# Optimization experiments

Hardware: AMD Instinct MI355X
Metric: run time of the kernel (lower is better)

The kernel has to match this reference:

```python
import jax, jax.numpy as jnp
import numpy as np

N = 50000      # num_nodes
E = 1000000    # graph edges
EP = 400000    # pos/neg link-pred edges
H = 128        # hidden_dim
C = 768        # chemical_dim
L = 2          # num GCN layers


def setup_inputs() -> dict:
    key = jax.random.key(0)
    ks = jax.random.split(key, 12)
    edge_index = jax.random.randint(ks[0], (2, E), 0, N)
    chemistry = jax.random.normal(ks[1], (N, C), jnp.float32)
    pos_edge = jax.random.randint(ks[2], (EP, 2), 0, N)
    neg_edge = jax.random.randint(ks[3], (EP, 2), 0, N)
    smiles_mask = jax.random.uniform(ks[4], (N,), jnp.float32)
    node_emb = jax.random.normal(ks[5], (N, H), jnp.float32) * 0.1
    conv_w = jax.random.normal(ks[6], (L, H, H), jnp.float32) / np.sqrt(H)
    conv_b = jnp.zeros((L, H), jnp.float32)
    chem_w = jax.random.normal(ks[7], (C, H), jnp.float32) / np.sqrt(C)
    chem_b = jnp.zeros((H,), jnp.float32)
    dec_w1 = jax.random.normal(ks[8], (2 * H, H), jnp.float32) / np.sqrt(2 * H)
    dec_b1 = jnp.zeros((H,), jnp.float32)
    dec_w2 = jax.random.normal(ks[9], (H, 1), jnp.float32) / np.sqrt(H)
    dec_b2 = jnp.zeros((1,), jnp.float32)
    return dict(edge_index=edge_index, chemistry=chemistry, pos_edge=pos_edge,
                neg_edge=neg_edge, smiles_mask=smiles_mask, node_emb=node_emb,
                conv_w=conv_w, conv_b=conv_b, chem_w=chem_w, chem_b=chem_b,
                dec_w1=dec_w1, dec_b1=dec_b1, dec_w2=dec_w2, dec_b2=dec_b2)


def reference(edge_index, chemistry, pos_edge, neg_edge, smiles_mask, node_emb,
              conv_w, conv_b, chem_w, chem_b, dec_w1, dec_b1, dec_w2, dec_b2):
    row, col = edge_index[0], edge_index[1]  # src -> dst
    # GCN symmetric normalization (add_self_loops=False)
    deg = jax.ops.segment_sum(jnp.ones((E,), jnp.float32), col, num_segments=N)
    dinv = jnp.where(deg > 0, 1.0 / jnp.sqrt(jnp.maximum(deg, 1.0)), 0.0)
    norm = dinv[row] * dinv[col]  # [E]

    # Encoder: structure-only GCN over learned node embeddings
    z = node_emb
    for l in range(L):
        h = z @ conv_w[l]                       # [N,H]
        msg = h[row] * norm[:, None]            # gather [E,H]
        agg = jax.ops.segment_sum(msg, col, num_segments=N)  # scatter-add
        z = jax.nn.relu(agg + conv_b[l])

    # Chemistry projection, masked by smiles validity
    c = jax.nn.relu(chemistry @ chem_w + chem_b) * smiles_mask[:, None]  # [N,H]

    def decode(edges):
        src, dst = edges[:, 0], edges[:, 1]
        f = jnp.concatenate([z[src] * z[dst], c[src] * c[dst]], axis=-1)  # [Ep,2H]
        hmid = jax.nn.relu(f @ dec_w1 + dec_b1)
        return (hmid @ dec_w2 + dec_b2)[:, 0]

    return decode(pos_edge), decode(neg_edge)
```

## Files before the change

### kernel.cpp

```cpp
#include <hip/hip_runtime.h>
#include <hip/hip_fp16.h>

#define NN 50000
#define NE 1000000
#define NEP 400000
#define HD 128
#define CD 768
#define NB_SCAN 196
#define FSTR 256
#define NBKT 196
#define PBLK 2048
#define NPB ((2 * NEP + PBLK - 1) / PBLK)

typedef _Float16 f16x8 __attribute__((ext_vector_type(8)));
typedef _Float16 f16x2 __attribute__((ext_vector_type(2)));
typedef __fp16 hf16x2 __attribute__((ext_vector_type(2)));
typedef __attribute__((ext_vector_type(4))) float f32x4;

__device__ __forceinline__ unsigned pk2h(float a, float b) {
    hf16x2 p = __builtin_amdgcn_cvt_pkrtz(a, b);
    return __builtin_bit_cast(unsigned, p);
}
__device__ __forceinline__ ushort f2h(float x) {
    return (ushort)(pk2h(x, 0.f) & 0xffffu);
}
__device__ __forceinline__ unsigned h2mul(unsigned a, unsigned b) {
    f16x2 ha = __builtin_bit_cast(f16x2, a);
    f16x2 hb = __builtin_bit_cast(f16x2, b);
    f16x2 r = ha * hb;
    return __builtin_bit_cast(unsigned, r);
}
__device__ __forceinline__ f16x8 pack8h(float4 a0, float4 a1) {
    union { unsigned u[4]; f16x8 v; } r;
    r.u[0] = pk2h(a0.x, a0.y);
    r.u[1] = pk2h(a0.z, a0.w);
    r.u[2] = pk2h(a1.x, a1.y);
    r.u[3] = pk2h(a1.z, a1.w);
    return r.v;
}
__device__ __forceinline__ float2 h2f2(unsigned u) {
    f16x2 h = __builtin_bit_cast(f16x2, u);
    return make_float2((float)h[0], (float)h[1]);
}

__global__ __launch_bounds__(256) void count_kernel(const int* __restrict__ col,
                                                    int* __restrict__ cnt) {
    int i = blockIdx.x * 256 + threadIdx.x;
    if (i < NE) atomicAdd(&cnt[col[i]], 1);
}

__global__ __launch_bounds__(256) void dinv_kernel(const int* __restrict__ cnt,
                                                   float* __restrict__ dinv) {
    int i = blockIdx.x * 256 + threadIdx.x;
    if (i < NN) {
        int d = cnt[i];
        dinv[i] = (d > 0) ? 1.0f / sqrtf((float)d) : 0.0f;
    }
}

__global__ __launch_bounds__(256) void scan1_kernel(const int* __restrict__ cnt,
                                                    int* __restrict__ partial,
                                                    int* __restrict__ bsum) {
    __shared__ int s[256];
    int i = blockIdx.x * 256 + threadIdx.x;
    int v = (i < NN) ? cnt[i] : 0;
    s[threadIdx.x] = v;
    __syncthreads();
    for (int o = 1; o < 256; o <<= 1) {
        int t = (threadIdx.x >= o) ? s[threadIdx.x - o] : 0;
        __syncthreads();
        s[threadIdx.x] += t;
        __syncthreads();
    }
    if (i < NN) partial[i] = s[threadIdx.x] - v;
    if (threadIdx.x == 255) bsum[blockIdx.x] = s[255];
}

__global__ __launch_bounds__(256) void scan2_kernel(int* __restrict__ bsum) {
    __shared__ int s[256];
    int v = (threadIdx.x < NB_SCAN) ? bsum[threadIdx.x] : 0;
    s[threadIdx.x] = v;
    __syncthreads();
    for (int o = 1; o < 256; o <<= 1) {
        int t = (threadIdx.x >= o) ? s[threadIdx.x - o] : 0;
        __syncthreads();
        s[threadIdx.x] += t;
        __syncthreads();
    }
    if (threadIdx.x < NB_SCAN) bsum[threadIdx.x] = s[threadIdx.x] - v;
}

__global__ __launch_bounds__(256) void scan3_kernel(const int* __restrict__ partial,
                                                    const int* __restrict__ bsum,
                                                    int* __restrict__ off,
                                                    int* __restrict__ cursor) {
    int i = blockIdx.x * 256 + threadIdx.x;
    if (i < NN) {
        int o = partial[i] + bsum[blockIdx.x];
        off[i] = o;
        cursor[i] = o;
    }
}

__global__ __launch_bounds__(256) void fill_kernel(const int* __restrict__ row,
                                                   const int* __restrict__ col,
                                                   const float* __restrict__ dinv,
                                                   int* __restrict__ cursor,
                                                   int* __restrict__ csr_idx,
                                                   float* __restrict__ csr_w) {
    int e = blockIdx.x * 256 + threadIdx.x;
    if (e < NE) {
        int c = col[e], r = row[e];
        int slot = atomicAdd(&cursor[c], 1);
        csr_idx[slot] = r;
        csr_w[slot] = dinv[r];
    }
}

__global__ __launch_bounds__(256) void ehist_kernel(const int* __restrict__ pos,
                                                    const int* __restrict__ neg,
                                                    int* __restrict__ bh,
                                                    int* __restrict__ bcnt) {
    __shared__ int h[NBKT];
    const int t = threadIdx.x;
    if (t < NBKT) h[t] = 0;
    __syncthreads();
    const int base = blockIdx.x * PBLK;
#pragma unroll
    for (int j = 0; j < 8; ++j) {
        int i = base + t + j * 256;
        if (i < 2 * NEP) {
            int s = (i < NEP) ? pos[2 * i] : neg[2 * (i - NEP)];
            atomicAdd(&h[s >> 8], 1);
        }
    }
    __syncthreads();
    if (t < NBKT) {
        bh[blockIdx.x * NBKT + t] = h[t];
        if (h[t]) atomicAdd(&bcnt[t], h[t]);
    }
}

__global__ __launch_bounds__(256) void escan_kernel(const int* __restrict__ bcnt,
                                                    int* __restrict__ base) {
    __shared__ int s[256];
    const int t = threadIdx.x;
    int v = (t < NBKT) ? bcnt[t] : 0;
    s[t] = v;
    __syncthreads();
    for (int o = 1; o < 256; o <<= 1) {
        int x = (t >= o) ? s[t - o] : 0;
        __syncthreads();
        s[t] += x;
        __syncthreads();
    }
    if (t < NBKT) base[t] = s[t] - v;
}

__global__ __launch_bounds__(256) void bscan_kernel(const int* __restrict__ bh,
                                                    int* __restrict__ obh) {
    __shared__ int p[256];
    const int b = blockIdx.x;
    const int t = threadIdx.x;
    int v0 = (2 * t < NPB) ? bh[(size_t)(2 * t) * NBKT + b] : 0;
    int v1 = (2 * t + 1 < NPB) ? bh[(size_t)(2 * t + 1) * NBKT + b] : 0;
    p[t] = v0 + v1;
    __syncthreads();
    for (int o = 1; o < 256; o <<= 1) {
        int x = (t >= o) ? p[t - o] : 0;
        __syncthreads();
        p[t] += x;
        __syncthreads();
    }
    int excl = (t > 0) ? p[t - 1] : 0;
    if (2 * t < NPB) obh[(size_t)(2 * t) * NBKT + b] = excl;
    if (2 * t + 1 < NPB) obh[(size_t)(2 * t + 1) * NBKT + b] = excl + v0;
}

__global__ __launch_bounds__(256) void epermute_kernel(const int* __restrict__ pos,
                                                       const int* __restrict__ neg,
                                                       const int* __restrict__ base,
                                                       const int* __restrict__ obh,
                                                       uint2* __restrict__ sd,
                                                       int* __restrict__ oidx) {
    __shared__ int cur[NBKT];
    const int t = threadIdx.x;
    if (t < NBKT) cur[t] = base[t] + obh[(size_t)blockIdx.x * NBKT + t];
    __syncthreads();
    const int bb = blockIdx.x * PBLK;
#pragma unroll
    for (int j = 0; j < 8; ++j) {
        int i = bb + t + j * 256;
        if (i < 2 * NEP) {
            int s, d;
            if (i < NEP) { s = pos[2 * i]; d = pos[2 * i + 1]; }
            else { s = neg[2 * (i - NEP)]; d = neg[2 * (i - NEP) + 1]; }
            int slot = atomicAdd(&cur[s >> 8], 1);
            sd[slot] = make_uint2((unsigned)s, (unsigned)d);
            oidx[slot] = i;
        }
    }
}

__global__ __launch_bounds__(256) void wfrag_kernel(const float* __restrict__ w,
                                                    ushort* __restrict__ wf) {
    int tid = blockIdx.x * 256 + threadIdx.x;
    int ks = tid >> 9, nt = (tid >> 6) & 7, l = tid & 63;
    int kbase = ks * 32 + ((l >> 4) << 3);
    int colq = nt * 16 + (l & 15);
    ushort r[8];
#pragma unroll
    for (int j = 0; j < 8; ++j) r[j] = f2h(w[(size_t)(kbase + j) * HD + colq]);
    *(uint4*)&wf[(size_t)tid * 8] = *(uint4*)r;
}

template <int KS, bool EPI>
__global__ __launch_bounds__(256) void feat_mfma_kernel(const float* __restrict__ A,
                                                        const ushort* __restrict__ wf,
                                                        const float* __restrict__ bias,
                                                        const float* __restrict__ mask,
                                                        ushort* __restrict__ out,
                                                        int ostride, int ooff) {
    __shared__ float At[64][36];
    const int t = threadIdx.x;
    const int w = t >> 6, lane = t & 63;
    const int rowBase = blockIdx.x * 64;
    const int nt0 = w * 2;
    const int K = KS * 32;

    f32x4 acc[4][2] = {};

    for (int ks = 0; ks < KS; ++ks) {
        __syncthreads();
#pragma unroll
        for (int i = 0; i < 2; ++i) {
            int li = t + i * 256;
            int r = li >> 3, c4 = li & 7;
            int grow = rowBase + r;
            float4 v = make_float4(0.f, 0.f, 0.f, 0.f);
            if (grow < NN) v = *(const float4*)&A[(size_t)grow * K + ks * 32 + c4 * 4];
            *(float4*)&At[r][c4 * 4] = v;
        }
        __syncthreads();
        f16x8 bf0 = ((const f16x8*)wf)[(ks * 8 + nt0) * 64 + lane];
        f16x8 bf1 = ((const f16x8*)wf)[(ks * 8 + nt0 + 1) * 64 + lane];
#pragma unroll
        for (int mt = 0; mt < 4; ++mt) {
            int row = mt * 16 + (lane & 15);
            float4 a0 = *(const float4*)&At[row][(lane >> 4) * 8];
            float4 a1 = *(const float4*)&At[row][(lane >> 4) * 8 + 4];
            f16x8 af = pack8h(a0, a1);
            acc[mt][0] = __builtin_amdgcn_mfma_f32_16x16x32_f16(af, bf0, acc[mt][0], 0, 0, 0);
            acc[mt][1] = __builtin_amdgcn_mfma_f32_16x16x32_f16(af, bf1, acc[mt][1], 0, 0, 0);
        }
    }

    const int c0 = lane & 15, rq = lane >> 4;
    float bb0 = EPI ? bias[nt0 * 16 + c0] : 0.f;
    float bb1 = EPI ? bias[nt0 * 16 + 16 + c0] : 0.f;
#pragma unroll
    for (int mt = 0; mt < 4; ++mt) {
#pragma unroll
        for (int reg = 0; reg < 4; ++reg) {
            int grow = rowBase + mt * 16 + rq * 4 + reg;
            if (grow < NN) {
                float v0 = acc[mt][0][reg], v1 = acc[mt][1][reg];
                if (EPI) {
                    float m = mask[grow];
                    v0 = fmaxf(v0 + bb0, 0.f) * m;
                    v1 = fmaxf(v1 + bb1, 0.f) * m;
                }
                out[(size_t)grow * ostride + ooff + nt0 * 16 + c0] = f2h(v0);
                out[(size_t)grow * ostride + ooff + nt0 * 16 + 16 + c0] = f2h(v1);
            }
        }
    }
}

template <bool F16OUT>
__global__ __launch_bounds__(256) void gather_kernel(const int* __restrict__ off,
                                                     const int* __restrict__ cnt,
                                                     const int* __restrict__ csr_idx,
                                                     const float* __restrict__ csr_w,
                                                     const float* __restrict__ dinv,
                                                     const ushort* __restrict__ h,
                                                     const float* __restrict__ bias,
                                                     float* __restrict__ z,
                                                     ushort* __restrict__ zb,
                                                     int ostride) {
    int v = blockIdx.x * 4 + (threadIdx.x >> 6);
    if (v >= NN) return;
    int lane = threadIdx.x & 63;
    int s = off[v];
    int e = s + cnt[v];
    float accx = 0.f, accy = 0.f;
    for (; s + 7 < e; s += 8) {
        int r0 = csr_idx[s], r1 = csr_idx[s + 1], r2 = csr_idx[s + 2], r3 = csr_idx[s + 3];
        int r4 = csr_idx[s + 4], r5 = csr_idx[s + 5], r6 = csr_idx[s + 6], r7 = csr_idx[s + 7];
        unsigned u0 = *(const unsigned*)&h[(size_t)r0 * HD + lane * 2];
        unsigned u1 = *(const unsigned*)&h[(size_t)r1 * HD + lane * 2];
        unsigned u2 = *(const unsigned*)&h[(size_t)r2 * HD + lane * 2];
        unsigned u3 = *(const unsigned*)&h[(size_t)r3 * HD + lane * 2];
        unsigned u4 = *(const unsigned*)&h[(size_t)r4 * HD + lane * 2];
        unsigned u5 = *(const unsigned*)&h[(size_t)r5 * HD + lane * 2];
        unsigned u6 = *(const unsigned*)&h[(size_t)r6 * HD + lane * 2];
        unsigned u7 = *(const unsigned*)&h[(size_t)r7 * HD + lane * 2];
        float w0 = csr_w[s], w1 = csr_w[s + 1], w2 = csr_w[s + 2], w3 = csr_w[s + 3];
        float w4 = csr_w[s + 4], w5 = csr_w[s + 5], w6 = csr_w[s + 6], w7 = csr_w[s + 7];
        float2 f0 = h2f2(u0), f1 = h2f2(u1), f2 = h2f2(u2), f3 = h2f2(u3);
        float2 f4 = h2f2(u4), f5 = h2f2(u5), f6 = h2f2(u6), f7 = h2f2(u7);
        accx = fmaf(f0.x, w0, accx); accy = fmaf(f0.y, w0, accy);
        accx = fmaf(f1.x, w1, accx); accy = fmaf(f1.y, w1, accy);
        accx = fmaf(f2.x, w2, accx); accy = fmaf(f2.y, w2, accy);
        accx = fmaf(f3.x, w3, accx); accy = fmaf(f3.y, w3, accy);
        accx = fmaf(f4.x, w4, accx); accy = fmaf(f4.y, w4, accy);
        accx = fmaf(f5.x, w5, accx); accy = fmaf(f5.y, w5, accy);
        accx = fmaf(f6.x, w6, accx); accy = fmaf(f6.y, w6, accy);
        accx = fmaf(f7.x, w7, accx); accy = fmaf(f7.y, w7, accy);
    }
    for (; s < e; ++s) {
        int r0 = csr_idx[s];
        float w0 = csr_w[s];
        float2 f0 = h2f2(*(const unsigned*)&h[(size_t)r0 * HD + lane * 2]);
        accx = fmaf(f0.x, w0, accx); accy = fmaf(f0.y, w0, accy);
    }
    float dv = dinv[v];
    float2 b = *(const float2*)&bias[lane * 2];
    float ox = fmaxf(fmaf(accx, dv, b.x), 0.f);
    float oy = fmaxf(fmaf(accy, dv, b.y), 0.f);
    if (F16OUT) {
        *(unsigned*)&zb[(size_t)v * ostride + lane * 2] = pk2h(ox, oy);
    } else {
        float2 o; o.x = ox; o.y = oy;
        *(float2*)&z[(size_t)v * HD + lane * 2] = o;
    }
}

__global__ __launch_bounds__(256, 4) void decode_mfma_kernel(const uint2* __restrict__ sedges,
                                                             const int* __restrict__ soidx,
                                                             const ushort* __restrict__ feat,
                                                             const ushort* __restrict__ w1f,
                                                             const float* __restrict__ b1,
                                                             const float* __restrict__ w2,
                                                             const float* __restrict__ b2,
                                                             float* __restrict__ out) {
    __shared__ ushort Flds[8 * 4 * 64 * 8];
    __shared__ int sEdge[128];
    __shared__ int sOut[64];
    __shared__ float part[4][64];
    const int t = threadIdx.x;
    const int w = t >> 6, lane = t & 63;

    const int nwg = gridDim.x;
    const int orig = blockIdx.x;
    const int q = nwg >> 3, r = nwg & 7;
    const int xcd = orig & 7, k = orig >> 3;
    const int wgid = (xcd < r ? xcd * (q + 1) : r * (q + 1) + (xcd - r) * q) + k;
    const int ebase = wgid * 64;

    if (t < 128) sEdge[t] = ((const int*)sedges)[(size_t)ebase * 2 + t];
    if (t < 64) sOut[t] = soidx[ebase + t];
    __syncthreads();

    const int seg = t & 31, eslot = t >> 5;
#pragma unroll
    for (int it = 0; it < 8; ++it) {
        int e = it * 8 + eslot;
        int s = sEdge[2 * e], dd = sEdge[2 * e + 1];
        uint4 av = *(const uint4*)&feat[(size_t)s * FSTR + seg * 8];
        uint4 bv = *(const uint4*)&feat[(size_t)dd * FSTR + seg * 8];
        uint4 res;
        res.x = h2mul(av.x, bv.x);
        res.y = h2mul(av.y, bv.y);
        res.z = h2mul(av.z, bv.z);
        res.w = h2mul(av.w, bv.w);
        int ks = seg >> 2;
        int mt = e >> 4;
        int fl = (e & 15) | ((seg & 3) << 4);
        int swz = (seg & 3) | ((ks & 1) << 2);
        ((uint4*)Flds)[(ks * 4 + mt) * 64 + (fl ^ swz)] = res;
    }
    __syncthreads();

    f32x4 acc[4][2] = {};
    const int nt0 = w * 2;
#pragma unroll
    for (int ks = 0; ks < 8; ++ks) {
        f16x8 bf0 = ((const f16x8*)w1f)[(ks * 8 + nt0) * 64 + lane];
        f16x8 bf1 = ((const f16x8*)w1f)[(ks * 8 + nt0 + 1) * 64 + lane];
        const int rswz = ((lane >> 4) & 3) | ((ks & 1) << 2);
#pragma unroll
        for (int mt = 0; mt < 4; ++mt) {
            f16x8 af = ((const f16x8*)Flds)[(ks * 4 + mt) * 64 + (lane ^ rswz)];
            acc[mt][0] = __builtin_amdgcn_mfma_f32_16x16x32_f16(af, bf0, acc[mt][0], 0, 0, 0);
            acc[mt][1] = __builtin_amdgcn_mfma_f32_16x16x32_f16(af, bf1, acc[mt][1], 0, 0, 0);
        }
    }

    const int c0 = lane & 15, rq = lane >> 4;
    float b1v0 = b1[nt0 * 16 + c0], b1v1 = b1[nt0 * 16 + 16 + c0];
    float w2v0 = w2[nt0 * 16 + c0], w2v1 = w2[nt0 * 16 + 16 + c0];
#pragma unroll
    for (int mt = 0; mt < 4; ++mt) {
#pragma unroll
        for (int reg = 0; reg < 4; ++reg) {
            float h0 = fmaxf(acc[mt][0][reg] + b1v0, 0.f);
            float h1 = fmaxf(acc[mt][1][reg] + b1v1, 0.f);
            float p = fmaf(h0, w2v0, h1 * w2v1);
            p += __shfl_xor(p, 1);
            p += __shfl_xor(p, 2);
            p += __shfl_xor(p, 4);
            p += __shfl_xor(p, 8);
            if (c0 == 0) part[w][mt * 16 + rq * 4 + reg] = p;
        }
    }
    __syncthreads();
    if (t < 64) {
        out[sOut[t]] = part[0][t] + part[1][t] + part[2][t] + part[3][t] + b2[0];
    }
}

extern "C" void kernel_launch(void* const* d_in, const int* in_sizes, int n_in,
                              void* d_out, int out_size, void* d_ws, size_t ws_size,
                              hipStream_t stream) {
    const int* edge_index = (const int*)d_in[0];
    const float* chemistry = (const float*)d_in[1];
    const int* pos_edge = (const int*)d_in[2];
    const int* neg_edge = (const int*)d_in[3];
    const float* smiles_mask = (const float*)d_in[4];
    const float* node_emb = (const float*)d_in[5];
    const float* conv_w = (const float*)d_in[6];
    const float* conv_b = (const float*)d_in[7];
    const float* chem_w = (const float*)d_in[8];
    const float* chem_b = (const float*)d_in[9];
    const float* dec_w1 = (const float*)d_in[10];
    const float* dec_b1 = (const float*)d_in[11];
    const float* dec_w2 = (const float*)d_in[12];
    const float* dec_b2 = (const float*)d_in[13];
    float* out = (float*)d_out;

    char* ws = (char*)d_ws;
    int* cnt = (int*)(ws + 0);
    float* dinv = (float*)(ws + 204800);
    int* partial = (int*)(ws + 409600);
    int* off = (int*)(ws + 614400);
    int* cursor = (int*)(ws + 819200);
    int* bsum = (int*)(ws + 1024000);
    int* bcnt = (int*)(ws + 1025024);
    int* bbase = (int*)(ws + 1026048);
    int* csr_idx = (int*)(ws + 1048576);
    float* csr_w = (float*)(ws + 5242880);
    float* bufZ = (float*)(ws + 9437184);
    ushort* hb = (ushort*)(ws + 35037184);
    ushort* feat = (ushort*)(ws + 47837184);
    ushort* w1f = (ushort*)(ws + 73437184);
    ushort* wcf = (ushort*)(ws + 73502720);
    ushort* wc0f = (ushort*)(ws + 73699328);
    ushort* wc1f = (ushort*)(ws + 73732096);
    uint2* sort_sd = (uint2*)(ws + 35037184);
    int* sort_oidx = (int*)(ws + 41437184);
    int* bh = (int*)(ws + 9437184);
    int* obh = (int*)(ws + 9857184);

    const int* e_row = edge_index;
    const int* e_col = edge_index + NE;

    hipMemsetAsync(cnt, 0, (size_t)NN * 4, stream);
    hipMemsetAsync(bcnt, 0, NBKT * 4, stream);
    count_kernel<<<(NE + 255) / 256, 256, 0, stream>>>(e_col, cnt);
    dinv_kernel<<<(NN + 255) / 256, 256, 0, stream>>>(cnt, dinv);
    scan1_kernel<<<NB_SCAN, 256, 0, stream>>>(cnt, partial, bsum);
    scan2_kernel<<<1, 256, 0, stream>>>(bsum);
    scan3_kernel<<<NB_SCAN, 256, 0, stream>>>(partial, bsum, off, cursor);
    fill_kernel<<<(NE + 255) / 256, 256, 0, stream>>>(e_row, e_col, dinv, cursor, csr_idx, csr_w);
    wfrag_kernel<<<16, 256, 0, stream>>>(dec_w1, w1f);
    wfrag_kernel<<<48, 256, 0, stream>>>(chem_w, wcf);
    wfrag_kernel<<<8, 256, 0, stream>>>(conv_w, wc0f);
    wfrag_kernel<<<8, 256, 0, stream>>>(conv_w + HD * HD, wc1f);

    const int mmGrid = (NN + 63) / 64;
    const int gaGrid = (NN + 3) / 4;

    feat_mfma_kernel<4, false><<<mmGrid, 256, 0, stream>>>(node_emb, wc0f, nullptr, nullptr, hb, HD, 0);
    gather_kernel<false><<<gaGrid, 256, 0, stream>>>(off, cnt, csr_idx, csr_w, dinv, hb, conv_b, bufZ, nullptr, 0);

    feat_mfma_kernel<4, false><<<mmGrid, 256, 0, stream>>>(bufZ, wc1f, nullptr, nullptr, hb, HD, 0);
    gather_kernel<true><<<gaGrid, 256, 0, stream>>>(off, cnt, csr_idx, csr_w, dinv, hb, conv_b + HD, nullptr, feat, FSTR);

    ehist_kernel<<<NPB, 256, 0, stream>>>(pos_edge, neg_edge, bh, bcnt);
    escan_kernel<<<1, 256, 0, stream>>>(bcnt, bbase);
    bscan_kernel<<<NBKT, 256, 0, stream>>>(bh, obh);
    epermute_kernel<<<NPB, 256, 0, stream>>>(pos_edge, neg_edge, bbase, obh, sort_sd, sort_oidx);

    feat_mfma_kernel<24, true><<<mmGrid, 256, 0, stream>>>(chemistry, wcf, chem_b, smiles_mask, feat, FSTR, HD);

    decode_mfma_kernel<<<2 * NEP / 64, 256, 0, stream>>>(sort_sd, sort_oidx, feat, w1f,
                                                         dec_b1, dec_w2, dec_b2, out);
}
```

Before: 452.7 us.

## Merge setup kernels, double-buffer feature GEMM loads, trim decode shared memory

Folds the dinv computation into the first scan kernel, merges the four weight-fragment conversions into one launch, and collapses two memsets into one by moving bcnt next to cnt. The feature GEMM now double-buffers its A tile in LDS and prefetches the next K-slice into registers, which removes one barrier per iteration. The decode kernel drops its shared edge and output-index staging, reads edges directly from global memory, reuses Flds for the partial sums, and raises its occupancy hint to 5. These aim to cut launch overhead and memory stalls, at the cost of more register pressure in decode and twice the LDS in the GEMM.

```diff
diff --git a/kernel.cpp b/kernel.cpp
--- a/kernel.cpp
+++ b/kernel.cpp
@@ -49,21 +49,14 @@
     if (i < NE) atomicAdd(&cnt[col[i]], 1);
 }
 
-__global__ __launch_bounds__(256) void dinv_kernel(const int* __restrict__ cnt,
-                                                   float* __restrict__ dinv) {
-    int i = blockIdx.x * 256 + threadIdx.x;
-    if (i < NN) {
-        int d = cnt[i];
-        dinv[i] = (d > 0) ? 1.0f / sqrtf((float)d) : 0.0f;
-    }
-}
-
 __global__ __launch_bounds__(256) void scan1_kernel(const int* __restrict__ cnt,
                                                     int* __restrict__ partial,
-                                                    int* __restrict__ bsum) {
+                                                    int* __restrict__ bsum,
+                                                    float* __restrict__ dinv) {
     __shared__ int s[256];
     int i = blockIdx.x * 256 + threadIdx.x;
     int v = (i < NN) ? cnt[i] : 0;
+    if (i < NN) dinv[i] = (v > 0) ? 1.0f / sqrtf((float)v) : 0.0f;
     s[threadIdx.x] = v;
     __syncthreads();
     for (int o = 1; o < 256; o <<= 1) {
@@ -202,16 +195,30 @@
     }
 }
 
-__global__ __launch_bounds__(256) void wfrag_kernel(const float* __restrict__ w,
-                                                    ushort* __restrict__ wf) {
+__global__ __launch_bounds__(256) void wfrag_all_kernel(const float* __restrict__ w1,
+                                                        const float* __restrict__ wc,
+                                                        const float* __restrict__ w0,
+                                                        const float* __restrict__ wl1,
+                                                        ushort* __restrict__ w1f,
+                                                        ushort* __restrict__ wcf,
+                                                        ushort* __restrict__ wc0f,
+                                                        ushort* __restrict__ wc1f) {
     int tid = blockIdx.x * 256 + threadIdx.x;
-    int ks = tid >> 9, nt = (tid >> 6) & 7, l = tid & 63;
+    int g = tid >> 9;
+    const float* w;
+    ushort* wf;
+    int ks;
+    if (g < 8) { w = w1; wf = w1f; ks = g; }
+    else if (g < 32) { w = wc; wf = wcf; ks = g - 8; }
+    else if (g < 36) { w = w0; wf = wc0f; ks = g - 32; }
+    else { w = wl1; wf = wc1f; ks = g - 36; }
+    int nt = (tid >> 6) & 7, l = tid & 63;
     int kbase = ks * 32 + ((l >> 4) << 3);
     int colq = nt * 16 + (l & 15);
     ushort r[8];
 #pragma unroll
     for (int j = 0; j < 8; ++j) r[j] = f2h(w[(size_t)(kbase + j) * HD + colq]);
-    *(uint4*)&wf[(size_t)tid * 8] = *(uint4*)r;
+    *(uint4*)&wf[(size_t)((ks * 8 + nt) * 64 + l) * 8] = *(uint4*)r;
 }
 
 template <int KS, bool EPI>
@@ -221,34 +228,39 @@
                                                         const float* __restrict__ mask,
                                                         ushort* __restrict__ out,
                                                         int ostride, int ooff) {
-    __shared__ float At[64][36];
+    __shared__ float At[2][64][36];
     const int t = threadIdx.x;
     const int w = t >> 6, lane = t & 63;
     const int rowBase = blockIdx.x * 64;
     const int nt0 = w * 2;
     const int K = KS * 32;
 
+    const int sr0 = t >> 3, sr1 = 32 + (t >> 3), sc4 = (t & 7) * 4;
+    const int g0 = rowBase + sr0, g1 = rowBase + sr1;
+
+    float4 p0 = make_float4(0.f, 0.f, 0.f, 0.f), p1 = p0;
+    if (g0 < NN) p0 = *(const float4*)&A[(size_t)g0 * K + sc4];
+    if (g1 < NN) p1 = *(const float4*)&A[(size_t)g1 * K + sc4];
+
     f32x4 acc[4][2] = {};
 
     for (int ks = 0; ks < KS; ++ks) {
-        __syncthreads();
-#pragma unroll
-        for (int i = 0; i < 2; ++i) {
-            int li = t + i * 256;
-            int r = li >> 3, c4 = li & 7;
-            int grow = rowBase + r;
-            float4 v = make_float4(0.f, 0.f, 0.f, 0.f);
-            if (grow < NN) v = *(const float4*)&A[(size_t)grow * K + ks * 32 + c4 * 4];
-            *(float4*)&At[r][c4 * 4] = v;
-        }
-        __syncthreads();
+        const int b = ks & 1;
+        *(float4*)&At[b][sr0][sc4] = p0;
+        *(float4*)&At[b][sr1][sc4] = p1;
+        __syncthreads();
+        if (ks + 1 < KS) {
+            p0 = make_float4(0.f, 0.f, 0.f, 0.f); p1 = p0;
+            if (g0 < NN) p0 = *(const float4*)&A[(size_t)g0 * K + (ks + 1) * 32 + sc4];
+            if (g1 < NN) p1 = *(const float4*)&A[(size_t)g1 * K + (ks + 1) * 32 + sc4];
+        }
         f16x8 bf0 = ((const f16x8*)wf)[(ks * 8 + nt0) * 64 + lane];
         f16x8 bf1 = ((const f16x8*)wf)[(ks * 8 + nt0 + 1) * 64 + lane];
 #pragma unroll
         for (int mt = 0; mt < 4; ++mt) {
             int row = mt * 16 + (lane & 15);
-            float4 a0 = *(const float4*)&At[row][(lane >> 4) * 8];
-            float4 a1 = *(const float4*)&At[row][(lane >> 4) * 8 + 4];
+            float4 a0 = *(const float4*)&At[b][row][(lane >> 4) * 8];
+            float4 a1 = *(const float4*)&At[b][row][(lane >> 4) * 8 + 4];
             f16x8 af = pack8h(a0, a1);
             acc[mt][0] = __builtin_amdgcn_mfma_f32_16x16x32_f16(af, bf0, acc[mt][0], 0, 0, 0);
             acc[mt][1] = __builtin_amdgcn_mfma_f32_16x16x32_f16(af, bf1, acc[mt][1], 0, 0, 0);
@@ -336,7 +348,7 @@
     }
 }
 
-__global__ __launch_bounds__(256, 4) void decode_mfma_kernel(const uint2* __restrict__ sedges,
+__global__ __launch_bounds__(256, 5) void decode_mfma_kernel(const uint2* __restrict__ sedges,
                                                              const int* __restrict__ soidx,
                                                              const ushort* __restrict__ feat,
                                                              const ushort* __restrict__ w1f,
@@ -345,9 +357,6 @@
                                                              const float* __restrict__ b2,
                                                              float* __restrict__ out) {
     __shared__ ushort Flds[8 * 4 * 64 * 8];
-    __shared__ int sEdge[128];
-    __shared__ int sOut[64];
-    __shared__ float part[4][64];
     const int t = threadIdx.x;
     const int w = t >> 6, lane = t & 63;
 
@@ -358,17 +367,13 @@
     const int wgid = (xcd < r ? xcd * (q + 1) : r * (q + 1) + (xcd - r) * q) + k;
     const int ebase = wgid * 64;
 
-    if (t < 128) sEdge[t] = ((const int*)sedges)[(size_t)ebase * 2 + t];
-    if (t < 64) sOut[t] = soidx[ebase + t];
-    __syncthreads();
-
     const int seg = t & 31, eslot = t >> 5;
 #pragma unroll
     for (int it = 0; it < 8; ++it) {
         int e = it * 8 + eslot;
-        int s = sEdge[2 * e], dd = sEdge[2 * e + 1];
-        uint4 av = *(const uint4*)&feat[(size_t)s * FSTR + seg * 8];
-        uint4 bv = *(const uint4*)&feat[(size_t)dd * FSTR + seg * 8];
+        uint2 sd = sedges[ebase + e];
+        uint4 av = *(const uint4*)&feat[(size_t)sd.x * FSTR + seg * 8];
+        uint4 bv = *(const uint4*)&feat[(size_t)sd.y * FSTR + seg * 8];
         uint4 res;
         res.x = h2mul(av.x, bv.x);
         res.y = h2mul(av.y, bv.y);
@@ -396,7 +401,9 @@
             acc[mt][1] = __builtin_amdgcn_mfma_f32_16x16x32_f16(af, bf1, acc[mt][1], 0, 0, 0);
         }
     }
-
+    __syncthreads();
+
+    float* partf = (float*)Flds;
     const int c0 = lane & 15, rq = lane >> 4;
     float b1v0 = b1[nt0 * 16 + c0], b1v1 = b1[nt0 * 16 + 16 + c0];
     float w2v0 = w2[nt0 * 16 + c0], w2v1 = w2[nt0 * 16 + 16 + c0];
@@ -411,12 +418,12 @@
             p += __shfl_xor(p, 2);
             p += __shfl_xor(p, 4);
             p += __shfl_xor(p, 8);
-            if (c0 == 0) part[w][mt * 16 + rq * 4 + reg] = p;
+            if (c0 == 0) partf[w * 64 + mt * 16 + rq * 4 + reg] = p;
         }
     }
     __syncthreads();
     if (t < 64) {
-        out[sOut[t]] = part[0][t] + part[1][t] + part[2][t] + part[3][t] + b2[0];
+        out[soidx[ebase + t]] = partf[t] + partf[64 + t] + partf[128 + t] + partf[192 + t] + b2[0];
     }
 }
 
@@ -441,12 +448,12 @@
 
     char* ws = (char*)d_ws;
     int* cnt = (int*)(ws + 0);
-    float* dinv = (float*)(ws + 204800);
+    int* bcnt = (int*)(ws + 204800);
+    float* dinv = (float*)(ws + 208896);
     int* partial = (int*)(ws + 409600);
     int* off = (int*)(ws + 614400);
     int* cursor = (int*)(ws + 819200);
     int* bsum = (int*)(ws + 1024000);
-    int* bcnt = (int*)(ws + 1025024);
     int* bbase = (int*)(ws + 1026048);
     int* csr_idx = (int*)(ws + 1048576);
     float* csr_w = (float*)(ws + 5242880);
@@ -465,18 +472,14 @@
     const int* e_row = edge_index;
     const int* e_col = edge_index + NE;
 
-    hipMemsetAsync(cnt, 0, (size_t)NN * 4, stream);
-    hipMemsetAsync(bcnt, 0, NBKT * 4, stream);
+    hipMemsetAsync(ws, 0, 205824, stream);
     count_kernel<<<(NE + 255) / 256, 256, 0, stream>>>(e_col, cnt);
-    dinv_kernel<<<(NN + 255) / 256, 256, 0, stream>>>(cnt, dinv);
-    scan1_kernel<<<NB_SCAN, 256, 0, stream>>>(cnt, partial, bsum);
+    scan1_kernel<<<NB_SCAN, 256, 0, stream>>>(cnt, partial, bsum, dinv);
     scan2_kernel<<<1, 256, 0, stream>>>(bsum);
     scan3_kernel<<<NB_SCAN, 256, 0, stream>>>(partial, bsum, off, cursor);
     fill_kernel<<<(NE + 255) / 256, 256, 0, stream>>>(e_row, e_col, dinv, cursor, csr_idx, csr_w);
-    wfrag_kernel<<<16, 256, 0, stream>>>(dec_w1, w1f);
-    wfrag_kernel<<<48, 256, 0, stream>>>(chem_w, wcf);
-    wfrag_kernel<<<8, 256, 0, stream>>>(conv_w, wc0f);
-    wfrag_kernel<<<8, 256, 0, stream>>>(conv_w + HD * HD, wc1f);
+    wfrag_all_kernel<<<80, 256, 0, stream>>>(dec_w1, chem_w, conv_w, conv_w + HD * HD,
+                                             w1f, wcf, wc0f, wc1f);
 
     const int mmGrid = (NN + 63) / 64;
     const int gaGrid = (NN + 3) / 4;
```

New measurement: 422.7 us. 6.6% less time.
